# Optimization experiments

Hardware: AMD Instinct MI355X
Metric: run time of the kernel (lower is better)

The kernel has to match this reference:

```python
import jax, jax.numpy as jnp
import numpy as np

NEG = -1000000000.0
EPS = 1e-05

def setup_inputs() -> dict:
    key = jax.random.key(0)
    k1, k2, k3, k4, k5 = jax.random.split(key, 5)
    B, L, E, Q = 64, 2048, 512, 256
    encoded_vecs = jax.random.normal(k1, (B, L, E), dtype=jnp.float32)
    query = jax.random.normal(k2, (B, Q), dtype=jnp.float32)
    length = jax.random.randint(k3, (B,), 1, L + 1, dtype=jnp.int32)
    # Xavier-normal-ish params
    W1 = jax.random.normal(k4, (E + Q, E), dtype=jnp.float32) * jnp.sqrt(2.0 / (E + Q + E))
    b1 = jnp.zeros((E,), dtype=jnp.float32)
    v = jax.random.normal(k5, (E,), dtype=jnp.float32) * jnp.sqrt(2.0 / (E + 1))
    return {"encoded_vecs": encoded_vecs, "query": query, "length": length,
            "W1": W1, "b1": b1, "v": v}

def reference(encoded_vecs, query, length, W1, b1, v):
    B, L, E = encoded_vecs.shape
    # broadcast 2D query over the length dim (repeat in torch code)
    q = jnp.broadcast_to(query[:, None, :], (B, L, query.shape[-1]))
    h = jnp.concatenate([encoded_vecs, q], axis=2)            # [B, L, E+Q]
    u = jnp.tanh(jnp.einsum('blc,ce->ble', h, W1) + b1)       # [B, L, E]
    logits = jnp.einsum('ble,e->bl', u, v)                    # [B, L]
    # masked softmax (faithful to masked_softmax in source)
    mask = (jnp.arange(L)[None, :] < length[:, None])         # [B, L] bool
    masked_logits = jnp.where(mask, logits, NEG)
    max_logits = jnp.max(masked_logits, axis=1, keepdims=True)
    exps = jnp.exp(masked_logits - max_logits) * mask.astype(logits.dtype)
    attention = exps / (jnp.sum(exps, axis=1, keepdims=True) + EPS)  # [B, L]
    context = jnp.einsum('bl,ble->be', attention, encoded_vecs)      # [B, E]
    return (context, attention)
```

## Files before the change

### kernel.cpp

```cpp
#include <hip/hip_runtime.h>

typedef __attribute__((ext_vector_type(4))) float float4v;
typedef __attribute__((ext_vector_type(2))) float float2v;
typedef __attribute__((ext_vector_type(8))) short short8;
typedef __attribute__((ext_vector_type(4))) float f32x4;

#define NEGV (-1000000000.0f)

#define MTOT (64 * 2048)

__device__ __forceinline__ unsigned short f2bf(float f) {
    unsigned int u = __float_as_uint(f);
    u += 0x7fffu + ((u >> 16) & 1u);
    return (unsigned short)(u >> 16);
}

__device__ __forceinline__ void gload_lds16(const void* g, void* l) {
    __builtin_amdgcn_global_load_lds(
        (__attribute__((address_space(1))) unsigned int*)(unsigned long long)(g),
        (__attribute__((address_space(3))) unsigned int*)(unsigned int)(unsigned long long)(l),
        16, 0, 0);
}

__global__ __launch_bounds__(256)
void prep_wt_kernel(const float* __restrict__ W1, unsigned short* __restrict__ Wt) {
    __shared__ float t[32][33];
    int bx = blockIdx.x & 15;
    int by = blockIdx.x >> 4;
    int tx = threadIdx.x & 31;
    int ty = threadIdx.x >> 5;
    #pragma unroll
    for (int i = 0; i < 4; ++i)
        t[ty + 8 * i][tx] = W1[(bx * 32 + ty + 8 * i) * 512 + by * 32 + tx];
    __syncthreads();
    #pragma unroll
    for (int i = 0; i < 4; ++i)
        Wt[(by * 32 + ty + 8 * i) * 512 + bx * 32 + tx] = f2bf(t[tx][ty + 8 * i]);
}

__global__ void prep_qc_kernel(const float* __restrict__ query, const float* __restrict__ W1,
                               const float* __restrict__ b1, float* __restrict__ qc) {
    int b = blockIdx.x;
    int e = threadIdx.x;
    float acc0 = b1[e];
    float acc1 = b1[e + 256];
    const float* w = W1 + 512 * 512;
    #pragma unroll 8
    for (int q = 0; q < 256; ++q) {
        float qv = query[b * 256 + q];
        acc0 += qv * w[q * 512 + e];
        acc1 += qv * w[q * 512 + e + 256];
    }
    qc[b * 512 + e] = acc0;
    qc[b * 512 + e + 256] = acc1;
}

__global__ __launch_bounds__(1024)
void gemm_logits_kernel(const float* __restrict__ A,
                        const unsigned short* __restrict__ Wt,
                        const float* __restrict__ qc,
                        const float* __restrict__ v,
                        const int* __restrict__ length,
                        float* __restrict__ logits)
{
    int bm = blockIdx.x;
    int b = bm >> 4;
    int l0 = (bm & 15) * 128;
    if (l0 >= length[b]) return;

    __shared__ unsigned short As[2][128 * 32];
    __shared__ unsigned short Bs[2][512 * 32];
    __shared__ float lred[128][8];

    int tid = threadIdx.x;
    int lane = tid & 63;
    int w = tid >> 6;
    int wm = w >> 3, wn = w & 7;
    long row0 = (long)bm * 128;

    int ar_r = tid >> 3;
    int ar_e = tid & 7;
    const char* gAr = (const char*)A + (row0 + ar_r) * 2048 + ar_e * 16;
    int awr = ar_r * 64 + ((ar_e * 8) ^ (((ar_r >> 1) & 3) << 4));

    int offw = w * 2048 + lane * 16;
    const char* gB0;
    const char* gB1;
    {
        int o = offw;
        int r = o >> 6;
        gB0 = (const char*)Wt + r * 1024 + ((o & 63) ^ (((r >> 1) & 3) << 4));
        o = offw + 1024;
        r = o >> 6;
        gB1 = (const char*)Wt + r * 1024 + ((o & 63) ^ (((r >> 1) & 3) << 4));
    }

    int aoff[4], boff[4];
    int kb = 16 * (lane >> 4);
    #pragma unroll
    for (int mi = 0; mi < 4; ++mi) {
        int ar = wm * 64 + (lane & 15) + mi * 16;
        aoff[mi] = ar * 64 + (kb ^ (((ar >> 1) & 3) << 4));
    }
    #pragma unroll
    for (int ni = 0; ni < 4; ++ni) {
        int br = wn * 64 + (lane & 15) + ni * 16;
        boff[ni] = br * 64 + (kb ^ (((br >> 1) & 3) << 4));
    }

    f32x4 acc[4][4] = {};
    float4v P;

#define GISSUE(t, sI) do {                                                   \
    P = *(const float4v*)(gAr + (t) * 128);                                  \
    char* lb_ = (char*)(&Bs[0][0]) + (sI) * 32768 + offw;                    \
    gload_lds16(gB0 + (t) * 64, lb_);                                        \
    gload_lds16(gB1 + (t) * 64, lb_ + 1024);                                 \
} while (0)

#define CVTW(sW) do {                                                        \
    union { unsigned int u[2]; unsigned long long ll; } pk_;                 \
    pk_.u[0] = (unsigned int)f2bf(P[0]) | ((unsigned int)f2bf(P[1]) << 16);  \
    pk_.u[1] = (unsigned int)f2bf(P[2]) | ((unsigned int)f2bf(P[3]) << 16);  \
    *(unsigned long long*)((char*)(&As[0][0]) + (sW) * 8192 + awr) = pk_.ll; \
} while (0)

#define KCOMP(sC) do {                                                       \
    const char* as_ = (const char*)(&As[0][0]) + (sC) * 8192;                \
    const char* bs_ = (const char*)(&Bs[0][0]) + (sC) * 32768;               \
    short8 af_[4];                                                           \
    _Pragma("unroll")                                                        \
    for (int mi = 0; mi < 4; ++mi) af_[mi] = *(const short8*)(as_ + aoff[mi]); \
    _Pragma("unroll")                                                        \
    for (int ni = 0; ni < 4; ++ni) {                                         \
        short8 bf_ = *(const short8*)(bs_ + boff[ni]);                       \
        _Pragma("unroll")                                                    \
        for (int mi = 0; mi < 4; ++mi)                                       \
            acc[mi][ni] = __builtin_amdgcn_mfma_f32_16x16x32_bf16(af_[mi], bf_, acc[mi][ni], 0, 0, 0); \
    }                                                                        \
} while (0)

#define KITER(t) do {                                                        \
    GISSUE((t) + 1, ((t) + 1) & 1);                                          \
    KCOMP((t) & 1);                                                          \
    asm volatile("s_waitcnt vmcnt(2)" ::: "memory");                         \
    CVTW(((t) + 1) & 1);                                                     \
    asm volatile("s_waitcnt vmcnt(0) lgkmcnt(0)" ::: "memory");              \
    __builtin_amdgcn_s_barrier();                                            \
    asm volatile("" ::: "memory");                                           \
} while (0)

    GISSUE(0, 0);
    asm volatile("s_waitcnt vmcnt(2)" ::: "memory");
    CVTW(0);
    asm volatile("s_waitcnt vmcnt(0) lgkmcnt(0)" ::: "memory");
    __builtin_amdgcn_s_barrier();
    asm volatile("" ::: "memory");

    KITER(0);  KITER(1);  KITER(2);  KITER(3);
    KITER(4);  KITER(5);  KITER(6);  KITER(7);
    KITER(8);  KITER(9);  KITER(10); KITER(11);
    KITER(12); KITER(13); KITER(14);
    KCOMP(1);

    const float* qcb = qc + b * 512;
    float vcol[4], qcol[4];
    #pragma unroll
    for (int ni = 0; ni < 4; ++ni) {
        int c = wn * 64 + ni * 16 + (lane & 15);
        vcol[ni] = v[c];
        qcol[ni] = qcb[c];
    }
    #pragma unroll
    for (int mi = 0; mi < 4; ++mi) {
        #pragma unroll
        for (int j2 = 0; j2 < 4; ++j2) {
            float s = 0.f;
            #pragma unroll
            for (int ni = 0; ni < 4; ++ni) {
                float xx = acc[mi][ni][j2] + qcol[ni];
                float e2 = __expf(2.0f * xx);
                float tt = 1.0f - 2.0f * __builtin_amdgcn_rcpf(e2 + 1.0f);
                s += tt * vcol[ni];
            }
            s += __shfl_xor(s, 1);
            s += __shfl_xor(s, 2);
            s += __shfl_xor(s, 4);
            s += __shfl_xor(s, 8);
            if ((lane & 15) == 0)
                lred[wm * 64 + mi * 16 + 4 * (lane >> 4) + j2][wn] = s;
        }
    }
    __syncthreads();
    if (tid < 128) {
        float lg = 0.f;
        #pragma unroll
        for (int q = 0; q < 8; ++q) lg += lred[tid][q];
        logits[row0 + tid] = lg;
    }
}

__global__ void softmax_kernel(const float* __restrict__ logits, const int* __restrict__ length,
                               float* __restrict__ att, float* __restrict__ ctx) {
    int b = blockIdx.x;
    int len = length[b];
    int tid = threadIdx.x;
    int lane = tid & 63, wv = tid >> 6;
    const float* p0 = logits + b * 2048;
    float* ab = att + b * 2048;

    ctx[b * 512 + tid] = 0.f;
    ctx[b * 512 + 256 + tid] = 0.f;

    float vals[8];
    float mymax = -3.402823466e38f;
    #pragma unroll
    for (int i = 0; i < 8; ++i) {
        int l = tid + i * 256;
        float xv = (l < len) ? p0[l] : NEGV;
        vals[i] = xv;
        mymax = fmaxf(mymax, xv);
    }
    #pragma unroll
    for (int m = 32; m; m >>= 1) mymax = fmaxf(mymax, __shfl_xor(mymax, m));
    __shared__ float sm[4];
    if (lane == 0) sm[wv] = mymax;
    __syncthreads();
    float bmax = fmaxf(fmaxf(sm[0], sm[1]), fmaxf(sm[2], sm[3]));

    float mysum = 0.f;
    #pragma unroll
    for (int i = 0; i < 8; ++i) {
        int l = tid + i * 256;
        float e = (l < len) ? __expf(vals[i] - bmax) : 0.f;
        vals[i] = e;
        mysum += e;
    }
    #pragma unroll
    for (int m = 32; m; m >>= 1) mysum += __shfl_xor(mysum, m);
    __shared__ float ss[4];
    if (lane == 0) ss[wv] = mysum;
    __syncthreads();
    float tot = ss[0] + ss[1] + ss[2] + ss[3];
    float inv = 1.0f / (tot + 1e-5f);
    #pragma unroll
    for (int i = 0; i < 8; ++i) {
        int l = tid + i * 256;
        ab[l] = vals[i] * inv;
    }
}

__global__ void ctx_kernel(const float* __restrict__ att, const float* __restrict__ enc,
                           const int* __restrict__ length, float* __restrict__ ctx) {
    int b = blockIdx.x;
    int lc = blockIdx.y;
    int len = length[b];
    int l0 = lc * 128;
    if (l0 >= len) return;
    int lim = len - l0;
    if (lim > 128) lim = 128;

    int t = threadIdx.x;
    const float* ab = att + b * 2048 + l0;
    const float* eb = enc + ((long)(b * 2048 + l0)) * 512 + t * 2;
    float c0 = 0.f, c1 = 0.f;
    #pragma unroll 4
    for (int l = 0; l < lim; ++l) {
        float a = ab[l];
        float2v e = *(const float2v*)(eb);
        eb += 512;
        c0 += a * e.x;
        c1 += a * e.y;
    }
    atomicAdd(&ctx[b * 512 + 2 * t], c0);
    atomicAdd(&ctx[b * 512 + 2 * t + 1], c1);
}

extern "C" void kernel_launch(void* const* d_in, const int* in_sizes, int n_in,
                              void* d_out, int out_size, void* d_ws, size_t ws_size,
                              hipStream_t stream) {
    const float* enc    = (const float*)d_in[0];
    const float* query  = (const float*)d_in[1];
    const int*   length = (const int*)d_in[2];
    const float* W1     = (const float*)d_in[3];
    const float* b1     = (const float*)d_in[4];
    const float* v      = (const float*)d_in[5];

    float* out = (float*)d_out;
    float* ctx = out;
    float* att = out + 64 * 512;

    char* ws = (char*)d_ws;
    float* logits      = (float*)ws;
    float* qc          = (float*)(ws + MTOT * 4);
    unsigned short* Wt = (unsigned short*)(ws + MTOT * 4 + 64 * 512 * 4);

    prep_wt_kernel<<<256, 256, 0, stream>>>(W1, Wt);
    prep_qc_kernel<<<64, 256, 0, stream>>>(query, W1, b1, qc);

    gemm_logits_kernel<<<1024, 1024, 0, stream>>>(enc, Wt, qc, v, length, logits);

    softmax_kernel<<<64, 256, 0, stream>>>(logits, length, att, ctx);

    dim3 g3(64, 16);
    ctx_kernel<<<g3, 256, 0, stream>>>(att, enc, length, ctx);
}
```

Measured before the change: 140.8 us.

## Fuse softmax numerator and context accumulation into GEMM epilogue

The GEMM epilogue now exponentiates the logits directly, with no max subtraction. It writes the unnormalized weights to att, atomically accumulates the per-batch sum, and computes a partial context from the encoder tile the block just processed, accumulating it with atomics. A small norm kernel then divides ctx and att by the sum, replacing the separate softmax and context kernels that re-read the encoder tensor from memory. Skipping the max is safe only while the logits stay small enough for fp32 exp; the logits are bounded by sum|v| because tanh is bounded. The change also adds global atomics on ctxraw and S.

```diff
diff --git a/kernel.cpp b/kernel.cpp
--- a/kernel.cpp
+++ b/kernel.cpp
@@ -39,9 +39,13 @@
 }
 
 __global__ void prep_qc_kernel(const float* __restrict__ query, const float* __restrict__ W1,
-                               const float* __restrict__ b1, float* __restrict__ qc) {
+                               const float* __restrict__ b1, float* __restrict__ qc,
+                               float* __restrict__ ctxraw, float* __restrict__ S) {
     int b = blockIdx.x;
     int e = threadIdx.x;
+    ctxraw[b * 512 + e] = 0.f;
+    ctxraw[b * 512 + 256 + e] = 0.f;
+    if (e == 0) S[b] = 0.f;
     float acc0 = b1[e];
     float acc1 = b1[e + 256];
     const float* w = W1 + 512 * 512;
@@ -56,21 +60,25 @@
 }
 
 __global__ __launch_bounds__(1024)
-void gemm_logits_kernel(const float* __restrict__ A,
-                        const unsigned short* __restrict__ Wt,
-                        const float* __restrict__ qc,
-                        const float* __restrict__ v,
-                        const int* __restrict__ length,
-                        float* __restrict__ logits)
+void gemm_fused_kernel(const float* __restrict__ A,
+                       const unsigned short* __restrict__ Wt,
+                       const float* __restrict__ qc,
+                       const float* __restrict__ v,
+                       const int* __restrict__ length,
+                       float* __restrict__ att,
+                       float* __restrict__ ctxraw,
+                       float* __restrict__ S)
 {
     int bm = blockIdx.x;
     int b = bm >> 4;
+    int len = length[b];
     int l0 = (bm & 15) * 128;
-    if (l0 >= length[b]) return;
+    if (l0 >= len) return;
 
     __shared__ unsigned short As[2][128 * 32];
     __shared__ unsigned short Bs[2][512 * 32];
     __shared__ float lred[128][8];
+    __shared__ float wbuf[128];
 
     int tid = threadIdx.x;
     int lane = tid & 63;
@@ -192,88 +200,50 @@
         }
     }
     __syncthreads();
+
     if (tid < 128) {
         float lg = 0.f;
         #pragma unroll
         for (int q = 0; q < 8; ++q) lg += lred[tid][q];
-        logits[row0 + tid] = lg;
-    }
-}
-
-__global__ void softmax_kernel(const float* __restrict__ logits, const int* __restrict__ length,
-                               float* __restrict__ att, float* __restrict__ ctx) {
+        float wf = (l0 + tid < len) ? __expf(lg) : 0.f;
+        att[row0 + tid] = wf;
+        wbuf[tid] = wf;
+        float s = wf;
+        #pragma unroll
+        for (int m = 32; m; m >>= 1) s += __shfl_xor(s, m);
+        if ((tid & 63) == 0) atomicAdd(&S[b], s);
+    }
+    __syncthreads();
+
+    {
+        int e = tid & 511;
+        int lh = tid >> 9;
+        const float* encb = A + (row0 + lh * 64) * 512 + e;
+        const float* wb = &wbuf[lh * 64];
+        float c = 0.f;
+        #pragma unroll 4
+        for (int l = 0; l < 64; ++l)
+            c += wb[l] * encb[l * 512];
+        atomicAdd(&ctxraw[b * 512 + e], c);
+    }
+}
+
+__global__ void norm_kernel(const float* __restrict__ S, const int* __restrict__ length,
+                            const float* __restrict__ ctxraw,
+                            float* __restrict__ att, float* __restrict__ ctx) {
     int b = blockIdx.x;
+    int tid = threadIdx.x;
+    float inv = 1.0f / S[b];
+    ctx[b * 512 + tid] = ctxraw[b * 512 + tid] * inv;
+    ctx[b * 512 + 256 + tid] = ctxraw[b * 512 + 256 + tid] * inv;
     int len = length[b];
-    int tid = threadIdx.x;
-    int lane = tid & 63, wv = tid >> 6;
-    const float* p0 = logits + b * 2048;
     float* ab = att + b * 2048;
-
-    ctx[b * 512 + tid] = 0.f;
-    ctx[b * 512 + 256 + tid] = 0.f;
-
-    float vals[8];
-    float mymax = -3.402823466e38f;
     #pragma unroll
     for (int i = 0; i < 8; ++i) {
         int l = tid + i * 256;
-        float xv = (l < len) ? p0[l] : NEGV;
-        vals[i] = xv;
-        mymax = fmaxf(mymax, xv);
-    }
-    #pragma unroll
-    for (int m = 32; m; m >>= 1) mymax = fmaxf(mymax, __shfl_xor(mymax, m));
-    __shared__ float sm[4];
-    if (lane == 0) sm[wv] = mymax;
-    __syncthreads();
-    float bmax = fmaxf(fmaxf(sm[0], sm[1]), fmaxf(sm[2], sm[3]));
-
-    float mysum = 0.f;
-    #pragma unroll
-    for (int i = 0; i < 8; ++i) {
-        int l = tid + i * 256;
-        float e = (l < len) ? __expf(vals[i] - bmax) : 0.f;
-        vals[i] = e;
-        mysum += e;
-    }
-    #pragma unroll
-    for (int m = 32; m; m >>= 1) mysum += __shfl_xor(mysum, m);
-    __shared__ float ss[4];
-    if (lane == 0) ss[wv] = mysum;
-    __syncthreads();
-    float tot = ss[0] + ss[1] + ss[2] + ss[3];
-    float inv = 1.0f / (tot + 1e-5f);
-    #pragma unroll
-    for (int i = 0; i < 8; ++i) {
-        int l = tid + i * 256;
-        ab[l] = vals[i] * inv;
-    }
-}
-
-__global__ void ctx_kernel(const float* __restrict__ att, const float* __restrict__ enc,
-                           const int* __restrict__ length, float* __restrict__ ctx) {
-    int b = blockIdx.x;
-    int lc = blockIdx.y;
-    int len = length[b];
-    int l0 = lc * 128;
-    if (l0 >= len) return;
-    int lim = len - l0;
-    if (lim > 128) lim = 128;
-
-    int t = threadIdx.x;
-    const float* ab = att + b * 2048 + l0;
-    const float* eb = enc + ((long)(b * 2048 + l0)) * 512 + t * 2;
-    float c0 = 0.f, c1 = 0.f;
-    #pragma unroll 4
-    for (int l = 0; l < lim; ++l) {
-        float a = ab[l];
-        float2v e = *(const float2v*)(eb);
-        eb += 512;
-        c0 += a * e.x;
-        c1 += a * e.y;
-    }
-    atomicAdd(&ctx[b * 512 + 2 * t], c0);
-    atomicAdd(&ctx[b * 512 + 2 * t + 1], c1);
+        float wv = ab[l];
+        ab[l] = (l < len) ? wv * inv : 0.f;
+    }
 }
 
 extern "C" void kernel_launch(void* const* d_in, const int* in_sizes, int n_in,
@@ -291,17 +261,15 @@
     float* att = out + 64 * 512;
 
     char* ws = (char*)d_ws;
-    float* logits      = (float*)ws;
-    float* qc          = (float*)(ws + MTOT * 4);
-    unsigned short* Wt = (unsigned short*)(ws + MTOT * 4 + 64 * 512 * 4);
+    float* qc          = (float*)ws;
+    unsigned short* Wt = (unsigned short*)(ws + 64 * 512 * 4);
+    float* ctxraw      = (float*)(ws + 64 * 512 * 4 + 512 * 1024);
+    float* S           = (float*)(ws + 64 * 512 * 4 + 512 * 1024 + 64 * 512 * 4);
 
     prep_wt_kernel<<<256, 256, 0, stream>>>(W1, Wt);
-    prep_qc_kernel<<<64, 256, 0, stream>>>(query, W1, b1, qc);
-
-    gemm_logits_kernel<<<1024, 1024, 0, stream>>>(enc, Wt, qc, v, length, logits);
-
-    softmax_kernel<<<64, 256, 0, stream>>>(logits, length, att, ctx);
-
-    dim3 g3(64, 16);
-    ctx_kernel<<<g3, 256, 0, stream>>>(att, enc, length, ctx);
-}
+    prep_qc_kernel<<<64, 256, 0, stream>>>(query, W1, b1, qc, ctxraw, S);
+
+    gemm_fused_kernel<<<1024, 1024, 0, stream>>>(enc, Wt, qc, v, length, att, ctxraw, S);
+
+    norm_kernel<<<64, 256, 0, stream>>>(S, length, ctxraw, att, ctx);
+}
```

Result: faster. 136.5 us (-3.1%).
